# Kernel optimization log

Measured on AMD Instinct MI355X. Metric: run time of the kernel, lower is better.

The kernel has to match this reference:

```python
import jax, jax.numpy as jnp
import numpy as np

L = 16          # quantization levels (MSB LUT)
UP = 2          # upscale factor
H, W = 2048, 2048

# neighbor offsets (x, y) for pixels b and c per kernel type: 'h', 'd', 'b'
_OFFSETS = [((0, 1), (0, 2)),   # h: horizontal
            ((1, 1), (2, 2)),   # d: diagonal
            ((1, 2), (2, 1))]   # b: anti-diagonal-ish


def setup_inputs() -> dict:
    key = jax.random.key(0)
    k1, k2 = jax.random.split(key)
    img_lr = jax.random.randint(k1, (H, W), 0, L, dtype=jnp.int32)
    msb_weight = jax.random.normal(k2, (3, L ** 3, UP * UP), dtype=jnp.float32)
    return {"img_lr": img_lr, "msb_weight": msb_weight}


def reference(img_lr, msb_weight):
    up = UP
    out = jnp.zeros((img_lr.shape[0] * up, img_lr.shape[1] * up), jnp.float32)
    for k in range(3):  # kernel types h, d, b
        (xb, yb), (xc, yc) = _OFFSETS[k]
        w = msb_weight[k]                         # [L^3, up*up]
        for r in range(4):                        # 4-fold rotation ensemble
            rot = jnp.rot90(img_lr, r)            # get_slice rotation
            dx, dy = rot.shape
            p = jnp.pad(rot, ((0, 2), (0, 2)), mode='reflect')
            a = p[:dx, :dy]                       # anchor pixel (0,0)
            b = p[xb:xb + dx, yb:yb + dy]
            c = p[xc:xc + dx, yc:yc + dy]
            idx = (a * (L * L) + b * L + c).reshape(-1)  # composite LUT index
            # gather, then interleave the up x up sub-pixels spatially
            tmp = w[idx].reshape(dx, dy, up, up)
            tmp = tmp.transpose(0, 2, 1, 3).reshape(dx * up, dy * up)
            out = out + jnp.rot90(tmp, (4 - r) % 4)      # rotate back
    return out / 3.0
```

## Files before the change

kernel.cpp:

```cpp
#include <hip/hip_runtime.h>
#include <hip/hip_fp16.h>

#define N 2048
#define ONW 4096
#define TW 128
#define TH 32
#define HW 132
#define HH 36
#define HELEMS (HW * HH)
#define LUT_ENTRIES 12288
#define LUT_BYTES (LUT_ENTRIES * 8)
#define SMEM_BYTES (LUT_BYTES + 2 * HELEMS * 4)

typedef _Float16 half4v __attribute__((ext_vector_type(4)));
typedef float fvec4 __attribute__((ext_vector_type(4)));

__device__ __forceinline__ int reflect(int i) {
    i = i < 0 ? -i : i;
    return i >= N ? 2 * N - 2 - i : i;
}

__constant__ int c_bo[3][2] = {{0, 1}, {1, 1}, {1, 2}};
__constant__ int c_co[3][2] = {{0, 2}, {2, 2}, {2, 1}};

__device__ __forceinline__ void calc_idx(const int n[6][6], int pi, int pj, int* idx)
{
    const int bo[3][2] = {{0, 1}, {1, 1}, {1, 2}};
    const int co[3][2] = {{0, 2}, {2, 2}, {2, 1}};
    const int a8 = n[2 + pi][2 + pj] << 8;
    #pragma unroll
    for (int r = 0; r < 4; ++r) {
        #pragma unroll
        for (int k = 0; k < 3; ++k) {
            const int bp = bo[k][0], bq = bo[k][1];
            const int cp = co[k][0], cq = co[k][1];
            const int bdi = (r == 0) ? bp : (r == 1) ? bq : (r == 2) ? -bp : -bq;
            const int bdj = (r == 0) ? bq : (r == 1) ? -bp : (r == 2) ? -bq : bp;
            const int cdi = (r == 0) ? cp : (r == 1) ? cq : (r == 2) ? -cp : -cq;
            const int cdj = (r == 0) ? cq : (r == 1) ? -cp : (r == 2) ? -cq : cp;
            const int bv = n[pi + 2 + bdi][pj + 2 + bdj];
            const int cv = n[pi + 2 + cdi][pj + 2 + cdj];
            idx[r * 3 + k] = (k * 4096 + a8) + (bv * 16 + cv);
        }
    }
}

__device__ __forceinline__ void consume(const half4v* v, float* o)
{
    #pragma unroll
    for (int r = 0; r < 4; ++r) {
        half4v S = v[3 * r] + v[3 * r + 1] + v[3 * r + 2];
        const float x = (float)S.x, y = (float)S.y;
        const float z = (float)S.z, w = (float)S.w;
        if (r == 0)      { o[0] += x; o[1] += y; o[2] += z; o[3] += w; }
        else if (r == 1) { o[0] += z; o[1] += x; o[2] += w; o[3] += y; }
        else if (r == 2) { o[0] += w; o[1] += z; o[2] += y; o[3] += x; }
        else             { o[0] += y; o[1] += w; o[2] += x; o[3] += z; }
    }
}

__global__ __launch_bounds__(1024, 4) void hdblut_kernel(
    const int* __restrict__ img, const float4* __restrict__ w4,
    float* __restrict__ out)
{
    extern __shared__ unsigned char smem[];
    half4v* lut = (half4v*)smem;
    int* bufs = (int*)(smem + LUT_BYTES);

    const int tx = threadIdx.x;
    const int ty = threadIdx.y;
    const int tid = ty * 64 + tx;
    const int x0 = (int)(blockIdx.x & 15) * TW;
    const int y0 = (int)(blockIdx.x >> 4) * (TH * 4);

    #pragma unroll
    for (int i = 0; i < 12; ++i) {
        int j = tid + i * 1024;
        float4 v = w4[j];
        half4v h;
        h.x = (_Float16)v.x; h.y = (_Float16)v.y;
        h.z = (_Float16)v.z; h.w = (_Float16)v.w;
        lut[j] = h;
    }

    for (int e = tid; e < HELEMS; e += 1024) {
        int rr = e / HW, cc = e - rr * HW;
        bufs[e] = img[reflect(y0 + rr - 2) * N + reflect(x0 + cc - 2)];
    }
    __syncthreads();

    const float s = 1.0f / 3.0f;
    fvec4* o4 = (fvec4*)out;

    int pre[5];
    #pragma unroll 1
    for (int t = 0; t < 4; ++t) {
        int* cur = bufs + (t & 1) * HELEMS;
        int* nxt = bufs + ((t + 1) & 1) * HELEMS;

        if (t < 3) {
            const int yb = y0 + (t + 1) * TH;
            #pragma unroll
            for (int u = 0; u < 5; ++u) {
                int e = tid + u * 1024;
                if (e < HELEMS) {
                    int rr = e / HW, cc = e - rr * HW;
                    pre[u] = img[reflect(yb + rr - 2) * N + reflect(x0 + cc - 2)];
                }
            }
        }

        int n[6][6];
        {
            const int r0 = 2 * ty, c0 = 2 * tx;
            #pragma unroll
            for (int r = 0; r < 6; ++r)
                #pragma unroll
                for (int j = 0; j < 3; ++j) {
                    int2 t2 = *(const int2*)&cur[(r0 + r) * HW + c0 + 2 * j];
                    n[r][2 * j] = t2.x; n[r][2 * j + 1] = t2.y;
                }
        }

        float acc[2][2][4];
        #pragma unroll
        for (int i = 0; i < 2; ++i)
            #pragma unroll
            for (int j = 0; j < 2; ++j)
                #pragma unroll
                for (int c = 0; c < 4; ++c) acc[i][j][c] = 0.f;

        {
            int idx[12];
            half4v vA[12], vB[12], vC[12], vD[12];

            calc_idx(n, 0, 0, idx);
            #pragma unroll
            for (int i = 0; i < 12; ++i) vA[i] = lut[idx[i]];
            __builtin_amdgcn_sched_group_barrier(0x100, 12, 0);

            calc_idx(n, 0, 1, idx);
            #pragma unroll
            for (int i = 0; i < 12; ++i) vB[i] = lut[idx[i]];
            __builtin_amdgcn_sched_group_barrier(0x100, 12, 0);

            consume(vA, acc[0][0]);

            calc_idx(n, 1, 0, idx);
            #pragma unroll
            for (int i = 0; i < 12; ++i) vC[i] = lut[idx[i]];
            __builtin_amdgcn_sched_group_barrier(0x100, 12, 0);

            consume(vB, acc[0][1]);

            calc_idx(n, 1, 1, idx);
            #pragma unroll
            for (int i = 0; i < 12; ++i) vD[i] = lut[idx[i]];
            __builtin_amdgcn_sched_group_barrier(0x100, 12, 0);

            consume(vC, acc[1][0]);
            consume(vD, acc[1][1]);
        }

        const int py = y0 + t * TH + 2 * ty;
        const int ox = (x0 + 2 * tx) * 2;
        {
            fvec4 v0 = {acc[0][0][0] * s, acc[0][0][1] * s, acc[0][1][0] * s, acc[0][1][1] * s};
            fvec4 v1 = {acc[0][0][2] * s, acc[0][0][3] * s, acc[0][1][2] * s, acc[0][1][3] * s};
            fvec4 v2 = {acc[1][0][0] * s, acc[1][0][1] * s, acc[1][1][0] * s, acc[1][1][1] * s};
            fvec4 v3 = {acc[1][0][2] * s, acc[1][0][3] * s, acc[1][1][2] * s, acc[1][1][3] * s};
            __builtin_nontemporal_store(v0, &o4[((2 * py + 0) * ONW + ox) >> 2]);
            __builtin_nontemporal_store(v1, &o4[((2 * py + 1) * ONW + ox) >> 2]);
            __builtin_nontemporal_store(v2, &o4[((2 * py + 2) * ONW + ox) >> 2]);
            __builtin_nontemporal_store(v3, &o4[((2 * py + 3) * ONW + ox) >> 2]);
        }

        if (t < 3) {
            #pragma unroll
            for (int u = 0; u < 5; ++u) {
                int e = tid + u * 1024;
                if (e < HELEMS) nxt[e] = pre[u];
            }
        }
        __syncthreads();
    }
}

extern "C" void kernel_launch(void* const* d_in, const int* in_sizes, int n_in,
                              void* d_out, int out_size, void* d_ws, size_t ws_size,
                              hipStream_t stream)
{
    const int* img = (const int*)d_in[0];
    const float4* w4 = (const float4*)d_in[1];
    float* out = (float*)d_out;
    (void)hipFuncSetAttribute(reinterpret_cast<const void*>(hdblut_kernel),
                              hipFuncAttributeMaxDynamicSharedMemorySize, SMEM_BYTES);
    hdblut_kernel<<<dim3(256), dim3(64, 16), SMEM_BYTES, stream>>>(img, w4, out);
}
```

Before: 91.79 us.

## Pre-convert LUT to fp16 in workspace and remap block order

Adds a small pre-kernel that converts the float LUT to fp16 once into the workspace buffer. Each of the 256 blocks then copies 96KB of fp16 instead of reading 192KB of fp32 and converting it. Block indices are also permuted (bid&7)<<5|bid>>3, presumably to spread neighbouring tiles across XCDs or improve L2 locality. The cost is an extra kernel launch and a dependency between the two kernels. The fallback path is used when no workspace is available.

```diff
diff --git a/kernel.cpp b/kernel.cpp
--- a/kernel.cpp
+++ b/kernel.cpp
@@ -20,9 +20,6 @@
     return i >= N ? 2 * N - 2 - i : i;
 }
 
-__constant__ int c_bo[3][2] = {{0, 1}, {1, 1}, {1, 2}};
-__constant__ int c_co[3][2] = {{0, 2}, {2, 2}, {2, 1}};
-
 __device__ __forceinline__ void calc_idx(const int n[6][6], int pi, int pj, int* idx)
 {
     const int bo[3][2] = {{0, 1}, {1, 1}, {1, 2}};
@@ -59,9 +56,21 @@
     }
 }
 
+__global__ __launch_bounds__(1024) void lut_convert_kernel(
+    const float4* __restrict__ w4, half4v* __restrict__ lut16)
+{
+    const int i = (int)blockIdx.x * 1024 + (int)threadIdx.x;
+    float4 v = w4[i];
+    half4v h;
+    h.x = (_Float16)v.x; h.y = (_Float16)v.y;
+    h.z = (_Float16)v.z; h.w = (_Float16)v.w;
+    lut16[i] = h;
+}
+
+template<bool PRE>
 __global__ __launch_bounds__(1024, 4) void hdblut_kernel(
     const int* __restrict__ img, const float4* __restrict__ w4,
-    float* __restrict__ out)
+    const float4* __restrict__ lut16g, float* __restrict__ out)
 {
     extern __shared__ unsigned char smem[];
     half4v* lut = (half4v*)smem;
@@ -70,17 +79,29 @@
     const int tx = threadIdx.x;
     const int ty = threadIdx.y;
     const int tid = ty * 64 + tx;
-    const int x0 = (int)(blockIdx.x & 15) * TW;
-    const int y0 = (int)(blockIdx.x >> 4) * (TH * 4);
-
-    #pragma unroll
-    for (int i = 0; i < 12; ++i) {
-        int j = tid + i * 1024;
-        float4 v = w4[j];
-        half4v h;
-        h.x = (_Float16)v.x; h.y = (_Float16)v.y;
-        h.z = (_Float16)v.z; h.w = (_Float16)v.w;
-        lut[j] = h;
+
+    const int bid = (int)blockIdx.x;
+    const int orig = ((bid & 7) << 5) | (bid >> 3);
+    const int x0 = (orig & 15) * TW;
+    const int y0 = (orig >> 4) * (TH * 4);
+
+    if (PRE) {
+        float4* lutf4 = (float4*)smem;
+        #pragma unroll
+        for (int i = 0; i < 6; ++i) {
+            int j = tid + i * 1024;
+            lutf4[j] = lut16g[j];
+        }
+    } else {
+        #pragma unroll
+        for (int i = 0; i < 12; ++i) {
+            int j = tid + i * 1024;
+            float4 v = w4[j];
+            half4v h;
+            h.x = (_Float16)v.x; h.y = (_Float16)v.y;
+            h.z = (_Float16)v.z; h.w = (_Float16)v.w;
+            lut[j] = h;
+        }
     }
 
     for (int e = tid; e < HELEMS; e += 1024) {
@@ -193,7 +214,17 @@
     const int* img = (const int*)d_in[0];
     const float4* w4 = (const float4*)d_in[1];
     float* out = (float*)d_out;
-    (void)hipFuncSetAttribute(reinterpret_cast<const void*>(hdblut_kernel),
-                              hipFuncAttributeMaxDynamicSharedMemorySize, SMEM_BYTES);
-    hdblut_kernel<<<dim3(256), dim3(64, 16), SMEM_BYTES, stream>>>(img, w4, out);
-}
+
+    if (d_ws != nullptr && ws_size >= (size_t)LUT_BYTES) {
+        (void)hipFuncSetAttribute(reinterpret_cast<const void*>(&hdblut_kernel<true>),
+                                  hipFuncAttributeMaxDynamicSharedMemorySize, SMEM_BYTES);
+        lut_convert_kernel<<<dim3(12), dim3(1024), 0, stream>>>(w4, (half4v*)d_ws);
+        hdblut_kernel<true><<<dim3(256), dim3(64, 16), SMEM_BYTES, stream>>>(
+            img, w4, (const float4*)d_ws, out);
+    } else {
+        (void)hipFuncSetAttribute(reinterpret_cast<const void*>(&hdblut_kernel<false>),
+                                  hipFuncAttributeMaxDynamicSharedMemorySize, SMEM_BYTES);
+        hdblut_kernel<false><<<dim3(256), dim3(64, 16), SMEM_BYTES, stream>>>(
+            img, w4, nullptr, out);
+    }
+}
```

After: 94.75 us. 1.03x slower.

## Load image neighborhoods directly from global memory, dropping LDS double-buffered halo

Applied to the files above, without the earlier changes.

Removes the shared-memory halo tile and its double-buffered prefetch, so each thread reads its 6x6 neighborhood straight from global memory (through cache). Interior threads use int2 vector loads and edge threads use per-element reflect indexing. This drops the per-iteration __syncthreads and the LDS halo space, leaving shared memory only for the LUT. In exchange there are redundant overlapping global reads (6x6 per 2x2 output block), a divergent edge path, and no explicit prefetch to overlap load latency with compute.

```diff
diff --git a/kernel.cpp b/kernel.cpp
--- a/kernel.cpp
+++ b/kernel.cpp
@@ -5,12 +5,9 @@
 #define ONW 4096
 #define TW 128
 #define TH 32
-#define HW 132
-#define HH 36
-#define HELEMS (HW * HH)
 #define LUT_ENTRIES 12288
 #define LUT_BYTES (LUT_ENTRIES * 8)
-#define SMEM_BYTES (LUT_BYTES + 2 * HELEMS * 4)
+#define SMEM_BYTES LUT_BYTES
 
 typedef _Float16 half4v __attribute__((ext_vector_type(4)));
 typedef float fvec4 __attribute__((ext_vector_type(4)));
@@ -19,9 +16,6 @@
     i = i < 0 ? -i : i;
     return i >= N ? 2 * N - 2 - i : i;
 }
-
-__constant__ int c_bo[3][2] = {{0, 1}, {1, 1}, {1, 2}};
-__constant__ int c_co[3][2] = {{0, 2}, {2, 2}, {2, 1}};
 
 __device__ __forceinline__ void calc_idx(const int n[6][6], int pi, int pj, int* idx)
 {
@@ -65,7 +59,6 @@
 {
     extern __shared__ unsigned char smem[];
     half4v* lut = (half4v*)smem;
-    int* bufs = (int*)(smem + LUT_BYTES);
 
     const int tx = threadIdx.x;
     const int ty = threadIdx.y;
@@ -82,44 +75,31 @@
         h.z = (_Float16)v.z; h.w = (_Float16)v.w;
         lut[j] = h;
     }
-
-    for (int e = tid; e < HELEMS; e += 1024) {
-        int rr = e / HW, cc = e - rr * HW;
-        bufs[e] = img[reflect(y0 + rr - 2) * N + reflect(x0 + cc - 2)];
-    }
     __syncthreads();
 
     const float s = 1.0f / 3.0f;
     fvec4* o4 = (fvec4*)out;
 
-    int pre[5];
+    const int c0 = x0 + 2 * tx - 2;
+    const bool fast = (c0 >= 0) && (c0 + 5 < N);
+
     #pragma unroll 1
     for (int t = 0; t < 4; ++t) {
-        int* cur = bufs + (t & 1) * HELEMS;
-        int* nxt = bufs + ((t + 1) & 1) * HELEMS;
-
-        if (t < 3) {
-            const int yb = y0 + (t + 1) * TH;
-            #pragma unroll
-            for (int u = 0; u < 5; ++u) {
-                int e = tid + u * 1024;
-                if (e < HELEMS) {
-                    int rr = e / HW, cc = e - rr * HW;
-                    pre[u] = img[reflect(yb + rr - 2) * N + reflect(x0 + cc - 2)];
-                }
-            }
-        }
-
+        const int ybase = y0 + t * TH + 2 * ty;
         int n[6][6];
-        {
-            const int r0 = 2 * ty, c0 = 2 * tx;
-            #pragma unroll
-            for (int r = 0; r < 6; ++r)
+        #pragma unroll
+        for (int r = 0; r < 6; ++r) {
+            const int* row = img + reflect(ybase - 2 + r) * N;
+            if (fast) {
                 #pragma unroll
                 for (int j = 0; j < 3; ++j) {
-                    int2 t2 = *(const int2*)&cur[(r0 + r) * HW + c0 + 2 * j];
+                    int2 t2 = *(const int2*)(row + c0 + 2 * j);
                     n[r][2 * j] = t2.x; n[r][2 * j + 1] = t2.y;
                 }
+            } else {
+                #pragma unroll
+                for (int j = 0; j < 6; ++j) n[r][j] = row[reflect(c0 + j)];
+            }
         }
 
         float acc[2][2][4];
@@ -162,7 +142,7 @@
             consume(vD, acc[1][1]);
         }
 
-        const int py = y0 + t * TH + 2 * ty;
+        const int py = ybase;
         const int ox = (x0 + 2 * tx) * 2;
         {
             fvec4 v0 = {acc[0][0][0] * s, acc[0][0][1] * s, acc[0][1][0] * s, acc[0][1][1] * s};
@@ -174,15 +154,6 @@
             __builtin_nontemporal_store(v2, &o4[((2 * py + 2) * ONW + ox) >> 2]);
             __builtin_nontemporal_store(v3, &o4[((2 * py + 3) * ONW + ox) >> 2]);
         }
-
-        if (t < 3) {
-            #pragma unroll
-            for (int u = 0; u < 5; ++u) {
-                int e = tid + u * 1024;
-                if (e < HELEMS) nxt[e] = pre[u];
-            }
-        }
-        __syncthreads();
     }
 }
 
```

Measured after the change: 102.9 us. 1.12x slower.

## Add atomic work-stealing scheduler with smaller tiles over persistent blocks

Applied to the files above, without the earlier changes.

Splits the image into 512 half-height work items and has each of the 256 blocks pull items from a global atomic counter, which is zeroed by an extra tiny kernel launched first. The aim is better load balance across CUs and less tail idling than the fixed one-tile-per-block mapping. In exchange, every item reloads its halo without overlap, adds two block barriers and an atomic per pull, and adds a second kernel launch. The nontemporal output stores are also replaced by plain stores.

```diff
diff --git a/kernel.cpp b/kernel.cpp
--- a/kernel.cpp
+++ b/kernel.cpp
@@ -10,7 +10,8 @@
 #define HELEMS (HW * HH)
 #define LUT_ENTRIES 12288
 #define LUT_BYTES (LUT_ENTRIES * 8)
-#define SMEM_BYTES (LUT_BYTES + 2 * HELEMS * 4)
+#define NITEMS 512
+#define SMEM_BYTES (LUT_BYTES + 2 * HELEMS * 4 + 16)
 
 typedef _Float16 half4v __attribute__((ext_vector_type(4)));
 typedef float fvec4 __attribute__((ext_vector_type(4)));
@@ -19,9 +20,6 @@
     i = i < 0 ? -i : i;
     return i >= N ? 2 * N - 2 - i : i;
 }
-
-__constant__ int c_bo[3][2] = {{0, 1}, {1, 1}, {1, 2}};
-__constant__ int c_co[3][2] = {{0, 2}, {2, 2}, {2, 1}};
 
 __device__ __forceinline__ void calc_idx(const int n[6][6], int pi, int pj, int* idx)
 {
@@ -59,19 +57,20 @@
     }
 }
 
+__global__ void zero_counter(unsigned* __restrict__ c) { *c = 0u; }
+
 __global__ __launch_bounds__(1024, 4) void hdblut_kernel(
     const int* __restrict__ img, const float4* __restrict__ w4,
-    float* __restrict__ out)
+    float* __restrict__ out, unsigned* __restrict__ cnt)
 {
     extern __shared__ unsigned char smem[];
     half4v* lut = (half4v*)smem;
     int* bufs = (int*)(smem + LUT_BYTES);
+    volatile int* s_item = (volatile int*)(smem + LUT_BYTES + 2 * HELEMS * 4);
 
     const int tx = threadIdx.x;
     const int ty = threadIdx.y;
     const int tid = ty * 64 + tx;
-    const int x0 = (int)(blockIdx.x & 15) * TW;
-    const int y0 = (int)(blockIdx.x >> 4) * (TH * 4);
 
     #pragma unroll
     for (int i = 0; i < 12; ++i) {
@@ -82,107 +81,126 @@
         h.z = (_Float16)v.z; h.w = (_Float16)v.w;
         lut[j] = h;
     }
-
-    for (int e = tid; e < HELEMS; e += 1024) {
-        int rr = e / HW, cc = e - rr * HW;
-        bufs[e] = img[reflect(y0 + rr - 2) * N + reflect(x0 + cc - 2)];
-    }
     __syncthreads();
 
     const float s = 1.0f / 3.0f;
     fvec4* o4 = (fvec4*)out;
 
-    int pre[5];
-    #pragma unroll 1
-    for (int t = 0; t < 4; ++t) {
-        int* cur = bufs + (t & 1) * HELEMS;
-        int* nxt = bufs + ((t + 1) & 1) * HELEMS;
-
-        if (t < 3) {
-            const int yb = y0 + (t + 1) * TH;
+    for (int pulls = 0; pulls < NITEMS; ++pulls) {
+        int item;
+        if (cnt != nullptr) {
+            if (tid == 0) *s_item = (int)atomicAdd(cnt, 1u);
+            __syncthreads();
+            item = *s_item;
+            __syncthreads();
+        } else {
+            if (pulls >= 2) break;
+            item = 2 * (int)blockIdx.x + pulls;
+            __syncthreads();
+        }
+        if ((unsigned)item >= NITEMS) break;
+
+        const int x0 = (item & 15) * TW;
+        const int y0 = (item >> 4) * (TH * 2);
+
+        for (int e = tid; e < HELEMS; e += 1024) {
+            int rr = e / HW, cc = e - rr * HW;
+            bufs[e] = img[reflect(y0 + rr - 2) * N + reflect(x0 + cc - 2)];
+        }
+        __syncthreads();
+
+        int pre[5];
+        #pragma unroll 1
+        for (int t = 0; t < 2; ++t) {
+            int* cur = bufs + (t & 1) * HELEMS;
+            int* nxt = bufs + ((t + 1) & 1) * HELEMS;
+
+            if (t < 1) {
+                const int yb = y0 + TH;
+                #pragma unroll
+                for (int u = 0; u < 5; ++u) {
+                    int e = tid + u * 1024;
+                    if (e < HELEMS) {
+                        int rr = e / HW, cc = e - rr * HW;
+                        pre[u] = img[reflect(yb + rr - 2) * N + reflect(x0 + cc - 2)];
+                    }
+                }
+            }
+
+            int n[6][6];
+            {
+                const int r0 = 2 * ty, c0 = 2 * tx;
+                #pragma unroll
+                for (int r = 0; r < 6; ++r)
+                    #pragma unroll
+                    for (int j = 0; j < 3; ++j) {
+                        int2 t2 = *(const int2*)&cur[(r0 + r) * HW + c0 + 2 * j];
+                        n[r][2 * j] = t2.x; n[r][2 * j + 1] = t2.y;
+                    }
+            }
+
+            float acc[2][2][4];
             #pragma unroll
-            for (int u = 0; u < 5; ++u) {
-                int e = tid + u * 1024;
-                if (e < HELEMS) {
-                    int rr = e / HW, cc = e - rr * HW;
-                    pre[u] = img[reflect(yb + rr - 2) * N + reflect(x0 + cc - 2)];
+            for (int i = 0; i < 2; ++i)
+                #pragma unroll
+                for (int j = 0; j < 2; ++j)
+                    #pragma unroll
+                    for (int c = 0; c < 4; ++c) acc[i][j][c] = 0.f;
+
+            {
+                int idx[12];
+                half4v vA[12], vB[12], vC[12], vD[12];
+
+                calc_idx(n, 0, 0, idx);
+                #pragma unroll
+                for (int i = 0; i < 12; ++i) vA[i] = lut[idx[i]];
+                __builtin_amdgcn_sched_group_barrier(0x100, 12, 0);
+
+                calc_idx(n, 0, 1, idx);
+                #pragma unroll
+                for (int i = 0; i < 12; ++i) vB[i] = lut[idx[i]];
+                __builtin_amdgcn_sched_group_barrier(0x100, 12, 0);
+
+                consume(vA, acc[0][0]);
+
+                calc_idx(n, 1, 0, idx);
+                #pragma unroll
+                for (int i = 0; i < 12; ++i) vC[i] = lut[idx[i]];
+                __builtin_amdgcn_sched_group_barrier(0x100, 12, 0);
+
+                consume(vB, acc[0][1]);
+
+                calc_idx(n, 1, 1, idx);
+                #pragma unroll
+                for (int i = 0; i < 12; ++i) vD[i] = lut[idx[i]];
+                __builtin_amdgcn_sched_group_barrier(0x100, 12, 0);
+
+                consume(vC, acc[1][0]);
+                consume(vD, acc[1][1]);
+            }
+
+            const int py = y0 + t * TH + 2 * ty;
+            const int ox = (x0 + 2 * tx) * 2;
+            {
+                fvec4 v0 = {acc[0][0][0] * s, acc[0][0][1] * s, acc[0][1][0] * s, acc[0][1][1] * s};
+                fvec4 v1 = {acc[0][0][2] * s, acc[0][0][3] * s, acc[0][1][2] * s, acc[0][1][3] * s};
+                fvec4 v2 = {acc[1][0][0] * s, acc[1][0][1] * s, acc[1][1][0] * s, acc[1][1][1] * s};
+                fvec4 v3 = {acc[1][0][2] * s, acc[1][0][3] * s, acc[1][1][2] * s, acc[1][1][3] * s};
+                o4[((2 * py + 0) * ONW + ox) >> 2] = v0;
+                o4[((2 * py + 1) * ONW + ox) >> 2] = v1;
+                o4[((2 * py + 2) * ONW + ox) >> 2] = v2;
+                o4[((2 * py + 3) * ONW + ox) >> 2] = v3;
+            }
+
+            if (t < 1) {
+                #pragma unroll
+                for (int u = 0; u < 5; ++u) {
+                    int e = tid + u * 1024;
+                    if (e < HELEMS) nxt[e] = pre[u];
                 }
-            }
-        }
-
-        int n[6][6];
-        {
-            const int r0 = 2 * ty, c0 = 2 * tx;
-            #pragma unroll
-            for (int r = 0; r < 6; ++r)
-                #pragma unroll
-                for (int j = 0; j < 3; ++j) {
-                    int2 t2 = *(const int2*)&cur[(r0 + r) * HW + c0 + 2 * j];
-                    n[r][2 * j] = t2.x; n[r][2 * j + 1] = t2.y;
-                }
-        }
-
-        float acc[2][2][4];
-        #pragma unroll
-        for (int i = 0; i < 2; ++i)
-            #pragma unroll
-            for (int j = 0; j < 2; ++j)
-                #pragma unroll
-                for (int c = 0; c < 4; ++c) acc[i][j][c] = 0.f;
-
-        {
-            int idx[12];
-            half4v vA[12], vB[12], vC[12], vD[12];
-
-            calc_idx(n, 0, 0, idx);
-            #pragma unroll
-            for (int i = 0; i < 12; ++i) vA[i] = lut[idx[i]];
-            __builtin_amdgcn_sched_group_barrier(0x100, 12, 0);
-
-            calc_idx(n, 0, 1, idx);
-            #pragma unroll
-            for (int i = 0; i < 12; ++i) vB[i] = lut[idx[i]];
-            __builtin_amdgcn_sched_group_barrier(0x100, 12, 0);
-
-            consume(vA, acc[0][0]);
-
-            calc_idx(n, 1, 0, idx);
-            #pragma unroll
-            for (int i = 0; i < 12; ++i) vC[i] = lut[idx[i]];
-            __builtin_amdgcn_sched_group_barrier(0x100, 12, 0);
-
-            consume(vB, acc[0][1]);
-
-            calc_idx(n, 1, 1, idx);
-            #pragma unroll
-            for (int i = 0; i < 12; ++i) vD[i] = lut[idx[i]];
-            __builtin_amdgcn_sched_group_barrier(0x100, 12, 0);
-
-            consume(vC, acc[1][0]);
-            consume(vD, acc[1][1]);
-        }
-
-        const int py = y0 + t * TH + 2 * ty;
-        const int ox = (x0 + 2 * tx) * 2;
-        {
-            fvec4 v0 = {acc[0][0][0] * s, acc[0][0][1] * s, acc[0][1][0] * s, acc[0][1][1] * s};
-            fvec4 v1 = {acc[0][0][2] * s, acc[0][0][3] * s, acc[0][1][2] * s, acc[0][1][3] * s};
-            fvec4 v2 = {acc[1][0][0] * s, acc[1][0][1] * s, acc[1][1][0] * s, acc[1][1][1] * s};
-            fvec4 v3 = {acc[1][0][2] * s, acc[1][0][3] * s, acc[1][1][2] * s, acc[1][1][3] * s};
-            __builtin_nontemporal_store(v0, &o4[((2 * py + 0) * ONW + ox) >> 2]);
-            __builtin_nontemporal_store(v1, &o4[((2 * py + 1) * ONW + ox) >> 2]);
-            __builtin_nontemporal_store(v2, &o4[((2 * py + 2) * ONW + ox) >> 2]);
-            __builtin_nontemporal_store(v3, &o4[((2 * py + 3) * ONW + ox) >> 2]);
-        }
-
-        if (t < 3) {
-            #pragma unroll
-            for (int u = 0; u < 5; ++u) {
-                int e = tid + u * 1024;
-                if (e < HELEMS) nxt[e] = pre[u];
-            }
-        }
-        __syncthreads();
+                __syncthreads();
+            }
+        }
     }
 }
 
@@ -193,7 +211,12 @@
     const int* img = (const int*)d_in[0];
     const float4* w4 = (const float4*)d_in[1];
     float* out = (float*)d_out;
+    unsigned* cnt = nullptr;
+    if (d_ws != nullptr && ws_size >= sizeof(unsigned)) {
+        cnt = (unsigned*)d_ws;
+        zero_counter<<<dim3(1), dim3(1), 0, stream>>>(cnt);
+    }
     (void)hipFuncSetAttribute(reinterpret_cast<const void*>(hdblut_kernel),
                               hipFuncAttributeMaxDynamicSharedMemorySize, SMEM_BYTES);
-    hdblut_kernel<<<dim3(256), dim3(64, 16), SMEM_BYTES, stream>>>(img, w4, out);
-}
+    hdblut_kernel<<<dim3(256), dim3(64, 16), SMEM_BYTES, stream>>>(img, w4, out, cnt);
+}
```

Measured after the change: 100.2 us. +9.2%, slower.
